# Optimization experiments

Hardware: AMD Instinct MI355X
Metric: run time of the kernel (lower is better)

The kernel has to match this reference:

```python
import jax, jax.numpy as jnp
import numpy as np

NUM_HEAD = 32
NUM_KV_HEAD = 8
HEAD_DIM = 128
EMBED_DIM = 4096
GROUP = NUM_HEAD // NUM_KV_HEAD + 2  # 6: 4 q slots + 1 k + 1 v
TOKENS = 64


def setup_inputs() -> dict:
    key = jax.random.key(0)
    k1, k2, k3 = jax.random.split(key, 3)
    inp = jax.random.normal(k1, (TOKENS, EMBED_DIM), dtype=jnp.float32)
    # fused GQA weight layout from load_parameter: [embed_dim, num_kv_head, group, head_dim]
    weight = jax.random.normal(k2, (EMBED_DIM, NUM_KV_HEAD, GROUP, HEAD_DIM), dtype=jnp.float32) * 0.02
    bias = jax.random.normal(k3, (NUM_KV_HEAD, GROUP, HEAD_DIM), dtype=jnp.float32) * 0.02
    return {"input": inp, "weight": weight, "bias": bias}


def reference(input, weight, bias):
    # fused grouped QKV GEMM (mm_qkv_group_out):
    # out[t, kv, g, d] = sum_e input[t, e] * weight[e, kv, g, d] + bias[kv, g, d]
    out = jnp.einsum('te,ekgd->tkgd', input, weight) + bias
    T = input.shape[0]
    q = out[:, :, : GROUP - 2, :].reshape(T, NUM_HEAD * HEAD_DIM)
    k = out[:, :, GROUP - 2, :].reshape(T, NUM_KV_HEAD * HEAD_DIM)
    v = out[:, :, GROUP - 1, :].reshape(T, NUM_KV_HEAD * HEAD_DIM)
    return (q, k, v)
```

## Files before the change

kernel.cpp:

```cpp
#include <hip/hip_runtime.h>


#define N_COLS 6144
#define K_DIM  4096
#define Q_SZ   (64 * 4096)
#define K_OFF  Q_SZ
#define V_OFF  (Q_SZ + 64 * 1024)
#define OUT_ELEMS 393216
#define IN_ELEMS  262144

typedef __bf16 bf16x8 __attribute__((ext_vector_type(8)));
typedef float  f32x4  __attribute__((ext_vector_type(4)));
typedef unsigned short us8 __attribute__((ext_vector_type(8)));

__device__ unsigned short g_abuf[IN_ELEMS];

__device__ __forceinline__ unsigned short f2bf_rne(float f) {
    unsigned int u = __float_as_uint(f);
    u += 0x7FFFu + ((u >> 16) & 1u);
    return (unsigned short)(u >> 16);
}

__device__ __forceinline__ int out_index(int t, int n) {
    const int kv = n / 768;
    const int g  = (n >> 7) % 6;
    const int d  = n & 127;
    if (g < 4)  return t * 4096 + kv * 512 + g * 128 + d;
    if (g == 4) return K_OFF + t * 1024 + kv * 128 + d;
    return V_OFF + t * 1024 + kv * 128 + d;
}

__global__ __launch_bounds__(256)
void init_kernel(const float* __restrict__ in, const float* __restrict__ bias,
                 float* __restrict__ out) {
    const int i = blockIdx.x * 256 + threadIdx.x;
    if (i < IN_ELEMS) g_abuf[i] = f2bf_rne(in[i]);
    if (i < OUT_ELEMS) {
        const int d   = i & 127;
        const int g   = (i >> 7) % 6;
        const int kvt = i / 768;
        const int kv  = kvt & 7;
        const int t   = kvt >> 3;
        out[out_index(t, kv * 768 + g * 128 + d)] = bias[(kv * 6 + g) * 128 + d];
    }
}

__global__ __launch_bounds__(256, 3)
void qkv_gemm(const float* __restrict__ w, float* __restrict__ out) {
    __shared__ float red[4][64][17];

    const int tid  = threadIdx.x;
    const int nt   = blockIdx.x >> 1;
    const int kh   = blockIdx.x & 1;
    const int n0   = nt * 16;
    const int wid  = tid >> 6;
    const int lane = tid & 63;
    const int l15  = lane & 15;
    const int kblk = lane >> 4;
    const int ks   = kh * 2048 + wid * 512;

    f32x4 acc[4] = {{0.f,0.f,0.f,0.f},{0.f,0.f,0.f,0.f},
                    {0.f,0.f,0.f,0.f},{0.f,0.f,0.f,0.f}};

    const float* bbase = w + (size_t)(ks + kblk * 8) * N_COLS + n0 + l15;
    const unsigned short* abase = g_abuf + l15 * K_DIM + ks + kblk * 8;

    #pragma unroll 4
    for (int kk = 0; kk < 512; kk += 32) {
        const float* bp = bbase + (size_t)kk * N_COLS;
        unsigned int b[8];
        #pragma unroll
        for (int j = 0; j < 8; ++j)
            b[j] = __float_as_uint(bp[(size_t)j * N_COLS]);

        us8 au0 = *(const us8*)(abase + kk);
        us8 au1 = *(const us8*)(abase + 16 * K_DIM + kk);
        us8 au2 = *(const us8*)(abase + 32 * K_DIM + kk);
        us8 au3 = *(const us8*)(abase + 48 * K_DIM + kk);

        union { unsigned int u[4]; us8 v; } pk;
        #pragma unroll
        for (int j = 0; j < 4; ++j) {
            const unsigned int lo = b[2 * j]     + 0x8000u;
            const unsigned int hi = b[2 * j + 1] + 0x8000u;
            pk.u[j] = (hi & 0xFFFF0000u) | (lo >> 16);
        }
        const bf16x8 bf = __builtin_bit_cast(bf16x8, pk.v);

        acc[0] = __builtin_amdgcn_mfma_f32_16x16x32_bf16(
                     __builtin_bit_cast(bf16x8, au0), bf, acc[0], 0, 0, 0);
        acc[1] = __builtin_amdgcn_mfma_f32_16x16x32_bf16(
                     __builtin_bit_cast(bf16x8, au1), bf, acc[1], 0, 0, 0);
        acc[2] = __builtin_amdgcn_mfma_f32_16x16x32_bf16(
                     __builtin_bit_cast(bf16x8, au2), bf, acc[2], 0, 0, 0);
        acc[3] = __builtin_amdgcn_mfma_f32_16x16x32_bf16(
                     __builtin_bit_cast(bf16x8, au3), bf, acc[3], 0, 0, 0);
    }

    #pragma unroll
    for (int tc = 0; tc < 4; ++tc)
        #pragma unroll
        for (int r = 0; r < 4; ++r)
            red[wid][lane][tc * 4 + r] = acc[tc][r];
    __syncthreads();

    const int l  = tid & 63;
    const int i0 = (tid >> 6) * 4;
    const int rl15  = l & 15;
    const int rkblk = l >> 4;
    #pragma unroll
    for (int r2 = 0; r2 < 4; ++r2) {
        const int i = i0 + r2;
        const float s = red[0][l][i] + red[1][l][i] + red[2][l][i] + red[3][l][i];
        const int tc = i >> 2, r = i & 3;
        const int t = tc * 16 + rkblk * 4 + r;
        atomicAdd(&out[out_index(t, n0 + rl15)], s);
    }
}

extern "C" void kernel_launch(void* const* d_in, const int* in_sizes, int n_in,
                              void* d_out, int out_size, void* d_ws, size_t ws_size,
                              hipStream_t stream) {
    const float* in   = (const float*)d_in[0];
    const float* w    = (const float*)d_in[1];
    const float* bias = (const float*)d_in[2];
    float* out = (float*)d_out;

    init_kernel<<<(OUT_ELEMS + 255) / 256, 256, 0, stream>>>(in, bias, out);
    qkv_gemm<<<768, 256, 0, stream>>>(w, out);
}
```

Measured before the change: 187.8 us.

## Pre-swizzle weights to bf16 MFMA layout and split K wider with direct atomics

Adds a pass that converts the fp32 weight into bf16 packed in the exact per-lane MFMA operand layout, using coalesced loads through LDS. The GEMM then reads one 16-byte vector per lane per step, prefetched one step ahead, instead of eight strided scalar loads with inline conversion. K is split 16 ways across blocks and the LDS reduction is removed, so each wave atomically adds its partials straight to the output. This trades extra memory traffic every call and many more atomics for far better-coalesced weight reads.

Measured after the change: 216.8 us. 15.4% more time.

```diff
diff --git a/kernel.cpp b/kernel.cpp
--- a/kernel.cpp
+++ b/kernel.cpp
@@ -11,14 +11,19 @@
 
 typedef __bf16 bf16x8 __attribute__((ext_vector_type(8)));
 typedef float  f32x4  __attribute__((ext_vector_type(4)));
-typedef unsigned short us8 __attribute__((ext_vector_type(8)));
+typedef unsigned int u32x4 __attribute__((ext_vector_type(4)));
 
 __device__ unsigned short g_abuf[IN_ELEMS];
+__device__ u32x4 g_wswz[384 * 128 * 64];
 
 __device__ __forceinline__ unsigned short f2bf_rne(float f) {
     unsigned int u = __float_as_uint(f);
     u += 0x7FFFu + ((u >> 16) & 1u);
     return (unsigned short)(u >> 16);
+}
+
+__device__ __forceinline__ unsigned int pack_pair(float lo, float hi) {
+    return ((unsigned int)f2bf_rne(hi) << 16) | f2bf_rne(lo);
 }
 
 __device__ __forceinline__ int out_index(int t, int n) {
@@ -45,77 +50,91 @@
     }
 }
 
-__global__ __launch_bounds__(256, 3)
-void qkv_gemm(const float* __restrict__ w, float* __restrict__ out) {
-    __shared__ float red[4][64][17];
+__global__ __launch_bounds__(256)
+void tswz(const float* __restrict__ w) {
+    __shared__ float Ls[32][256];
 
-    const int tid  = threadIdx.x;
-    const int nt   = blockIdx.x >> 1;
-    const int kh   = blockIdx.x & 1;
-    const int n0   = nt * 16;
-    const int wid  = tid >> 6;
+    const int bid = blockIdx.x;
+    const int n0  = (bid % 24) * 256;
+    const int ks  = bid / 24;
+    const int k0  = ks * 32;
+    const int tid = threadIdx.x;
+
+    #pragma unroll
+    for (int i = 0; i < 8; ++i) {
+        const int slot = i * 256 + tid;
+        const int row  = slot >> 6;
+        const int col4 = slot & 63;
+        *(float4*)&Ls[row][col4 * 4] =
+            *(const float4*)(w + (size_t)(k0 + row) * N_COLS + n0 + col4 * 4);
+    }
+    __syncthreads();
+
     const int lane = tid & 63;
     const int l15  = lane & 15;
     const int kblk = lane >> 4;
-    const int ks   = kh * 2048 + wid * 512;
+    #pragma unroll
+    for (int p = 0; p < 4; ++p) {
+        const int ci = p * 4 + (tid >> 6);
+        const int n  = ci * 16 + l15;
+        u32x4 cell;
+        #pragma unroll
+        for (int j2 = 0; j2 < 4; ++j2) {
+            const int k2 = kblk * 8 + 2 * j2;
+            cell[j2] = pack_pair(Ls[k2][n], Ls[k2 + 1][n]);
+        }
+        const int nt = (n0 >> 4) + ci;
+        g_wswz[(((size_t)nt * 128 + ks) << 6) + lane] = cell;
+    }
+}
+
+__global__ __launch_bounds__(256, 6)
+void qkv_gemm(float* __restrict__ out) {
+    const int tid  = threadIdx.x;
+    const int bid  = blockIdx.x;
+    const int nt   = bid >> 2;
+    const int wid  = tid >> 6;
+    const int kq   = (bid & 3) * 4 + wid;
+    const int lane = tid & 63;
+    const int l15  = lane & 15;
+    const int kblk = lane >> 4;
+
+    const u32x4* bp = &g_wswz[(((size_t)nt * 128 + kq * 8) << 6) + lane];
+    const unsigned short* ab = g_abuf + l15 * K_DIM + kq * 256 + kblk * 8;
 
     f32x4 acc[4] = {{0.f,0.f,0.f,0.f},{0.f,0.f,0.f,0.f},
                     {0.f,0.f,0.f,0.f},{0.f,0.f,0.f,0.f}};
 
-    const float* bbase = w + (size_t)(ks + kblk * 8) * N_COLS + n0 + l15;
-    const unsigned short* abase = g_abuf + l15 * K_DIM + ks + kblk * 8;
+    u32x4 bcur = bp[0];
+    #pragma unroll
+    for (int s = 0; s < 8; ++s) {
+        u32x4 bnext;
+        if (s < 7) bnext = bp[(s + 1) << 6];
 
-    #pragma unroll 4
-    for (int kk = 0; kk < 512; kk += 32) {
-        const float* bp = bbase + (size_t)kk * N_COLS;
-        unsigned int b[8];
-        #pragma unroll
-        for (int j = 0; j < 8; ++j)
-            b[j] = __float_as_uint(bp[(size_t)j * N_COLS]);
+        const unsigned short* ap = ab + s * 32;
+        const u32x4 a0 = *(const u32x4*)(ap);
+        const u32x4 a1 = *(const u32x4*)(ap + 16 * K_DIM);
+        const u32x4 a2 = *(const u32x4*)(ap + 32 * K_DIM);
+        const u32x4 a3 = *(const u32x4*)(ap + 48 * K_DIM);
 
-        us8 au0 = *(const us8*)(abase + kk);
-        us8 au1 = *(const us8*)(abase + 16 * K_DIM + kk);
-        us8 au2 = *(const us8*)(abase + 32 * K_DIM + kk);
-        us8 au3 = *(const us8*)(abase + 48 * K_DIM + kk);
-
-        union { unsigned int u[4]; us8 v; } pk;
-        #pragma unroll
-        for (int j = 0; j < 4; ++j) {
-            const unsigned int lo = b[2 * j]     + 0x8000u;
-            const unsigned int hi = b[2 * j + 1] + 0x8000u;
-            pk.u[j] = (hi & 0xFFFF0000u) | (lo >> 16);
-        }
-        const bf16x8 bf = __builtin_bit_cast(bf16x8, pk.v);
-
+        const bf16x8 bf = __builtin_bit_cast(bf16x8, bcur);
         acc[0] = __builtin_amdgcn_mfma_f32_16x16x32_bf16(
-                     __builtin_bit_cast(bf16x8, au0), bf, acc[0], 0, 0, 0);
+                     __builtin_bit_cast(bf16x8, a0), bf, acc[0], 0, 0, 0);
         acc[1] = __builtin_amdgcn_mfma_f32_16x16x32_bf16(
-                     __builtin_bit_cast(bf16x8, au1), bf, acc[1], 0, 0, 0);
+                     __builtin_bit_cast(bf16x8, a1), bf, acc[1], 0, 0, 0);
         acc[2] = __builtin_amdgcn_mfma_f32_16x16x32_bf16(
-                     __builtin_bit_cast(bf16x8, au2), bf, acc[2], 0, 0, 0);
+                     __builtin_bit_cast(bf16x8, a2), bf, acc[2], 0, 0, 0);
         acc[3] = __builtin_amdgcn_mfma_f32_16x16x32_bf16(
-                     __builtin_bit_cast(bf16x8, au3), bf, acc[3], 0, 0, 0);
+                     __builtin_bit_cast(bf16x8, a3), bf, acc[3], 0, 0, 0);
+        bcur = bnext;
     }
 
+    const int n = nt * 16 + l15;
     #pragma unroll
-    for (int tc = 0; tc < 4; ++tc)
+    for (int t16 = 0; t16 < 4; ++t16)
         #pragma unroll
         for (int r = 0; r < 4; ++r)
-            red[wid][lane][tc * 4 + r] = acc[tc][r];
-    __syncthreads();
-
-    const int l  = tid & 63;
-    const int i0 = (tid >> 6) * 4;
-    const int rl15  = l & 15;
-    const int rkblk = l >> 4;
-    #pragma unroll
-    for (int r2 = 0; r2 < 4; ++r2) {
-        const int i = i0 + r2;
-        const float s = red[0][l][i] + red[1][l][i] + red[2][l][i] + red[3][l][i];
-        const int tc = i >> 2, r = i & 3;
-        const int t = tc * 16 + rkblk * 4 + r;
-        atomicAdd(&out[out_index(t, n0 + rl15)], s);
-    }
+            atomicAdd(&out[out_index(t16 * 16 + kblk * 4 + r, n)], acc[t16][r]);
 }
 
 extern "C" void kernel_launch(void* const* d_in, const int* in_sizes, int n_in,
@@ -127,5 +146,6 @@
     float* out = (float*)d_out;
 
     init_kernel<<<(OUT_ELEMS + 255) / 256, 256, 0, stream>>>(in, bias, out);
-    qkv_gemm<<<768, 256, 0, stream>>>(w, out);
+    tswz<<<3072, 256, 0, stream>>>(w);
+    qkv_gemm<<<1536, 256, 0, stream>>>(out);
 }
```
